# Kernel tuning notes

Measured on AMD Instinct MI355X. Metric: run time of the kernel, lower is better.

The kernel has to match this reference:

```python
import jax, jax.numpy as jnp
import numpy as np

N = 50000      # nodes
E = 1600000    # edges (before self loops)
F = 128        # input_dim
H = 4          # num_heads
D = 32         # hidden_dim (per head)
B = 16         # graphs in batch
NEG_SLOPE = 0.2  # PyG GATv2Conv default negative_slope


def setup_inputs() -> dict:
    key = jax.random.key(0)
    ks = jax.random.split(key, 8)
    x = jax.random.normal(ks[0], (N, F), dtype=jnp.float32)
    edge_index = jax.random.randint(ks[1], (2, E), 0, N, dtype=jnp.int32)
    batch = jnp.sort(jax.random.randint(ks[2], (N,), 0, B, dtype=jnp.int32))
    s = 0.05
    W_l = jax.random.normal(ks[3], (F, H * D), dtype=jnp.float32) * s
    b_l = jnp.zeros((H * D,), dtype=jnp.float32)
    W_r = jax.random.normal(ks[4], (F, H * D), dtype=jnp.float32) * s
    b_r = jnp.zeros((H * D,), dtype=jnp.float32)
    att = jax.random.normal(ks[5], (H, D), dtype=jnp.float32) * s
    bias = jnp.zeros((H * D,), dtype=jnp.float32)
    return {"x": x, "edge_index": edge_index, "batch": batch,
            "W_l": W_l, "b_l": b_l, "W_r": W_r, "b_r": b_r,
            "att": att, "bias": bias}


def reference(x, edge_index, batch, W_l, b_l, W_r, b_r, att, bias):
    n = x.shape[0]
    # PyG GATv2Conv adds self loops by default
    loops = jnp.arange(n, dtype=edge_index.dtype)
    src = jnp.concatenate([edge_index[0], loops])  # message source j
    dst = jnp.concatenate([edge_index[1], loops])  # message target i

    xl = (x @ W_l + b_l).reshape(n, H, D)  # source transform
    xr = (x @ W_r + b_r).reshape(n, H, D)  # target transform

    # per-edge GATv2 attention logits: a^T LeakyReLU(xl_j + xr_i)
    m = xl[src] + xr[dst]                                   # [E+N, H, D]
    e = jnp.sum(jax.nn.leaky_relu(m, NEG_SLOPE) * att, -1)  # [E+N, H]

    # softmax over incoming edges of each destination node
    e_max = jax.ops.segment_max(e, dst, num_segments=n)
    ex = jnp.exp(e - e_max[dst])
    den = jax.ops.segment_sum(ex, dst, num_segments=n)
    alpha = ex / den[dst]                                   # [E+N, H]

    # weighted scatter-sum aggregation of source features
    out = jax.ops.segment_sum(alpha[..., None] * xl[src], dst, num_segments=n)
    out = out.reshape(n, H * D) + bias                      # concat heads + bias
    out = jax.nn.relu(out)

    # global max pool over nodes of each graph
    pooled = jax.ops.segment_max(out, batch, num_segments=B)
    pooled = jnp.where(jnp.isfinite(pooled), pooled, 0.0)   # guard empty graphs
    return pooled
```

## Files before the change

### kernel.cpp

```cpp
#include <hip/hip_runtime.h>

#define NN 50000
#define NE 1600000
#define FDIM 128
#define CDIM 128
#define NGRAPH 16
#define SLOPE 0.2f
#define CSTRIDE 96
#define BINSH 7
#define NBIN 391
#define EPB 6400
#define NB1 250
#define EPT 25
#define CAP 5120
#define POOL_NODES 64
#define POOL_NB ((NN + POOL_NODES - 1) / POOL_NODES)
#define TNB 782

__device__ __forceinline__ unsigned short f2bf(float f) {
    unsigned u = __float_as_uint(f);
    return (unsigned short)((u + 0x7FFFu + ((u >> 16) & 1u)) >> 16);
}
__device__ __forceinline__ unsigned packbf(float a, float b) {
    return (unsigned)f2bf(a) | ((unsigned)f2bf(b) << 16);
}
#define BFLO(u) __uint_as_float((u) << 16)
#define BFHI(u) __uint_as_float((u) & 0xffff0000u)

typedef __attribute__((ext_vector_type(8))) short short8;
typedef __attribute__((ext_vector_type(4))) float f32x4;
union FragU { uint4 u; short8 s; };

__global__ __launch_bounds__(256) void k_init(float* __restrict__ out,
                                              int* __restrict__ gbin_cnt) {
    int i = blockIdx.x * 256 + threadIdx.x;
    if (i < NGRAPH * CDIM) out[i] = 0.f;
    if (i < NBIN) gbin_cnt[i] = 0;
}

__global__ __launch_bounds__(256) void k_front(
    const float* __restrict__ x,
    const float* __restrict__ Wl, const float* __restrict__ bl,
    const float* __restrict__ Wr, const float* __restrict__ br,
    const int* __restrict__ src, const int* __restrict__ dst,
    int* __restrict__ gbin_cnt, unsigned* __restrict__ gstage,
    unsigned short* __restrict__ xlh, float* __restrict__ xr) {
    __shared__ __align__(16) char shraw[32768];
    const int tid = threadIdx.x;

    if (blockIdx.x < NB1) {
        int* bcnt = (int*)shraw;
        int* boff = bcnt + NBIN;
        int* gb   = boff + NBIN;
        int* sc   = gb + NBIN;
        unsigned* st = (unsigned*)(sc + 256);
        const int t  = tid;
        const int e0 = blockIdx.x * EPB;

        for (int b = t; b < NBIN; b += 256) bcnt[b] = 0;
        __syncthreads();

        unsigned sd[EPT]; int bn[EPT]; int pl[EPT];
#pragma unroll
        for (int k = 0; k < EPT; k++) {
            int e = e0 + k * 256 + t;
            int s = src[e], d = dst[e];
            bn[k] = d >> BINSH;
            sd[k] = (unsigned)s | ((unsigned)(d & 127) << 16)
                                | ((unsigned)bn[k] << 23);
            pl[k] = atomicAdd(&bcnt[bn[k]], 1);
        }
        __syncthreads();

        int c0 = (2*t     < NBIN) ? bcnt[2*t]     : 0;
        int c1 = (2*t + 1 < NBIN) ? bcnt[2*t + 1] : 0;
        int v  = c0 + c1;
        sc[t] = v; __syncthreads();
        for (int off = 1; off < 256; off <<= 1) {
            int add = (t >= off) ? sc[t - off] : 0;
            __syncthreads();
            sc[t] += add;
            __syncthreads();
        }
        int base = sc[t] - v;
        if (2*t     < NBIN) boff[2*t]     = base;
        if (2*t + 1 < NBIN) boff[2*t + 1] = base + c0;
        __syncthreads();

        for (int b = t; b < NBIN; b += 256) {
            int c = bcnt[b];
            gb[b] = (c > 0) ? atomicAdd(&gbin_cnt[b], c) : 0;
        }
#pragma unroll
        for (int k = 0; k < EPT; k++) st[boff[bn[k]] + pl[k]] = sd[k];
        __syncthreads();

        for (int idx = t; idx < EPB; idx += 256) {
            unsigned w = st[idx];
            int b = w >> 23;
            int p = gb[b] + (idx - boff[b]);
            if (p < CAP) gstage[(size_t)b * CAP + p] = w;
        }
    } else {
        uint4* wfrag = (uint4*)shraw;
        const int bid   = blockIdx.x - NB1;
        const int wv    = tid >> 6;
        const int lane  = tid & 63;
        const int quad  = lane >> 4;
        const int col   = lane & 15;
        const int node0 = bid * 64;
        const int nodeA = node0 + wv * 16 + col;
        const bool aval = nodeA < NN;

        FragU afrag[4];
#pragma unroll
        for (int kq = 0; kq < 4; kq++) {
            float4 lo = make_float4(0.f,0.f,0.f,0.f), hi = lo;
            if (aval) {
                const float* ap = &x[(size_t)nodeA * FDIM + kq * 32 + quad * 8];
                lo = *(const float4*)ap;
                hi = *(const float4*)(ap + 4);
            }
            afrag[kq].u.x = packbf(lo.x, lo.y);
            afrag[kq].u.y = packbf(lo.z, lo.w);
            afrag[kq].u.z = packbf(hi.x, hi.y);
            afrag[kq].u.w = packbf(hi.z, hi.w);
        }

        const int myrow0 = node0 + wv * 16 + quad * 4;

        for (int mat = 0; mat < 2; mat++) {
            const float* W  = mat ? Wr : Wl;
            const float* bb = mat ? br : bl;
            __syncthreads();
            for (int i = 0; i < 8; i++) {
                int C = i * 256 + tid;
                int ccol = C & 15, cq = (C >> 4) & 3, ckq = (C >> 6) & 3, cnt_ = C >> 8;
                const float* wp = &W[(size_t)(ckq * 32 + cq * 8) * CDIM + cnt_ * 16 + ccol];
                uint4 u;
                u.x = packbf(wp[0],        wp[CDIM]);
                u.y = packbf(wp[2*CDIM],   wp[3*CDIM]);
                u.z = packbf(wp[4*CDIM],   wp[5*CDIM]);
                u.w = packbf(wp[6*CDIM],   wp[7*CDIM]);
                wfrag[C] = u;
            }
            __syncthreads();

#pragma unroll
            for (int nt = 0; nt < 8; nt++) {
                f32x4 acc = {0.f, 0.f, 0.f, 0.f};
#pragma unroll
                for (int kq = 0; kq < 4; kq++) {
                    FragU bfr;
                    bfr.u = wfrag[(nt * 4 + kq) * 64 + lane];
                    acc = __builtin_amdgcn_mfma_f32_16x16x32_bf16(
                              afrag[kq].s, bfr.s, acc, 0, 0, 0);
                }
                int ch = nt * 16 + col;
                float bv = bb[ch];
                if (mat == 0) {
#pragma unroll
                    for (int r = 0; r < 4; r++) {
                        int node = myrow0 + r;
                        if (node < NN)
                            xlh[(size_t)node * CDIM + ch] = f2bf(acc[r] + bv);
                    }
                } else {
#pragma unroll
                    for (int r = 0; r < 4; r++) {
                        int node = myrow0 + r;
                        if (node < NN)
                            xr[(size_t)node * CDIM + ch] = acc[r] + bv;
                    }
                }
            }
        }
    }
}

__global__ __launch_bounds__(512) void k_csr(
    const int* __restrict__ gbin_cnt, const unsigned* __restrict__ gstage,
    int* __restrict__ cnt, unsigned short* __restrict__ colp) {
    __shared__ int nfill[128];
    __shared__ unsigned short crow[128 * CSTRIDE];
    const int bin = blockIdx.x;
    const int t   = threadIdx.x;
    const int n0  = bin << BINSH;
    const int nb  = min(128, NN - n0);
    const int m   = min(gbin_cnt[bin], CAP);

    if (t < 128) nfill[t] = 0;
    __syncthreads();

    unsigned w[10];
    bool     ok[10];
#pragma unroll
    for (int k = 0; k < 10; k++) {
        int i = k * 512 + t;
        ok[k] = i < m;
        if (ok[k]) w[k] = gstage[(size_t)bin * CAP + i];
    }
#pragma unroll
    for (int k = 0; k < 10; k++) {
        if (ok[k]) {
            int dl = (w[k] >> 16) & 127;
            int p  = atomicAdd(&nfill[dl], 1);
            if (p < CSTRIDE - 1)
                crow[dl * CSTRIDE + p] = (unsigned short)(w[k] & 0xFFFF);
        }
    }
    __syncthreads();

    if (t < nb) {
        int c = min(nfill[t], CSTRIDE - 1);
        crow[t * CSTRIDE + c] = (unsigned short)(n0 + t);
        cnt[n0 + t] = c + 1;
    }
    __syncthreads();

    unsigned* gout = (unsigned*)colp + (size_t)bin * (128 * CSTRIDE / 2);
    const unsigned* cin = (const unsigned*)crow;
    for (int idx = t; idx < 128 * CSTRIDE / 2; idx += 512) gout[idx] = cin[idx];
}

__device__ __forceinline__ void edge_body(
    const unsigned short* __restrict__ xlh, int j, int ch0,
    const float4& rx0, const float4& rx1,
    const float4& p0, const float4& p1,
    const float4& q0, const float4& q1,
    float& s, float* acc) {
    uint4 q = *(const uint4*)&xlh[(size_t)j * CDIM + ch0];
    float4 v0 = make_float4(BFLO(q.x), BFHI(q.x), BFLO(q.y), BFHI(q.y));
    float4 v1 = make_float4(BFLO(q.z), BFHI(q.z), BFLO(q.w), BFHI(q.w));
    float t0, d = 0.f;
    t0 = v0.x + rx0.x; d = fmaf(t0, p0.x, d); d = fmaf(fabsf(t0), q0.x, d);
    t0 = v0.y + rx0.y; d = fmaf(t0, p0.y, d); d = fmaf(fabsf(t0), q0.y, d);
    t0 = v0.z + rx0.z; d = fmaf(t0, p0.z, d); d = fmaf(fabsf(t0), q0.z, d);
    t0 = v0.w + rx0.w; d = fmaf(t0, p0.w, d); d = fmaf(fabsf(t0), q0.w, d);
    t0 = v1.x + rx1.x; d = fmaf(t0, p1.x, d); d = fmaf(fabsf(t0), q1.x, d);
    t0 = v1.y + rx1.y; d = fmaf(t0, p1.y, d); d = fmaf(fabsf(t0), q1.y, d);
    t0 = v1.z + rx1.z; d = fmaf(t0, p1.z, d); d = fmaf(fabsf(t0), q1.z, d);
    t0 = v1.w + rx1.w; d = fmaf(t0, p1.w, d); d = fmaf(fabsf(t0), q1.w, d);
    d += __shfl_xor(d, 1);
    d += __shfl_xor(d, 2);
    float w = __expf(d);
    s += w;
    acc[0] = fmaf(w, v0.x, acc[0]);
    acc[1] = fmaf(w, v0.y, acc[1]);
    acc[2] = fmaf(w, v0.z, acc[2]);
    acc[3] = fmaf(w, v0.w, acc[3]);
    acc[4] = fmaf(w, v1.x, acc[4]);
    acc[5] = fmaf(w, v1.y, acc[5]);
    acc[6] = fmaf(w, v1.z, acc[6]);
    acc[7] = fmaf(w, v1.w, acc[7]);
}

__global__ __launch_bounds__(256) void k_aggregate(
    const unsigned short* __restrict__ xlh, const float* __restrict__ xr,
    const float* __restrict__ att, const float* __restrict__ bias,
    const int* __restrict__ cnt, const unsigned short* __restrict__ colp,
    float* __restrict__ nodeout) {
    const int wave = blockIdx.x * 4 + (threadIdx.x >> 6);
    const int lane = threadIdx.x & 63;
    const int i     = wave;
    const size_t start = (size_t)i * CSTRIDE;
    const int deg   = cnt[i];
    const int grp   = lane >> 4;
    const int ch0   = (lane & 15) * 8;

    int cj0 = (int)colp[start + lane];
    int cj1 = 0;
    if (deg > 64) cj1 = (int)colp[start + 64 + lane];

    const float4 rx0 = *(const float4*)&xr[(size_t)i * CDIM + ch0];
    const float4 rx1 = *(const float4*)&xr[(size_t)i * CDIM + ch0 + 4];
    const float4 aa0 = *(const float4*)&att[ch0];
    const float4 aa1 = *(const float4*)&att[ch0 + 4];
    const float4 p0 = make_float4(0.6f*aa0.x, 0.6f*aa0.y, 0.6f*aa0.z, 0.6f*aa0.w);
    const float4 p1 = make_float4(0.6f*aa1.x, 0.6f*aa1.y, 0.6f*aa1.z, 0.6f*aa1.w);
    const float4 q0 = make_float4(0.4f*aa0.x, 0.4f*aa0.y, 0.4f*aa0.z, 0.4f*aa0.w);
    const float4 q1 = make_float4(0.4f*aa1.x, 0.4f*aa1.y, 0.4f*aa1.z, 0.4f*aa1.w);

    float s = 0.f;
    float acc[8];
#pragma unroll
    for (int k = 0; k < 8; k++) acc[k] = 0.f;

    const int full = deg >> 2;
    const int f0   = full < 16 ? full : 16;
#pragma unroll 2
    for (int t = 0; t < f0; t++) {
        int j = __shfl(cj0, t * 4 + grp);
        edge_body(xlh, j, ch0, rx0, rx1, p0, p1, q0, q1, s, acc);
    }
    for (int t = 16; t < full; t++) {
        int j = __shfl(cj1, t * 4 + grp - 64);
        edge_body(xlh, j, ch0, rx0, rx1, p0, p1, q0, q1, s, acc);
    }
    int e  = full * 4 + grp;
    int jt = (e < 64) ? __shfl(cj0, e) : __shfl(cj1, (e - 64) & 63);
    if (e < deg)
        edge_body(xlh, jt, ch0, rx0, rx1, p0, p1, q0, q1, s, acc);

#pragma unroll
    for (int dist = 16; dist <= 32; dist <<= 1) {
        s += __shfl_xor(s, dist);
#pragma unroll
        for (int k = 0; k < 8; k++) acc[k] += __shfl_xor(acc[k], dist);
    }

    if (grp == 0) {
        float inv = 1.f / s;
        float4 o0, o1;
        const float4 b0 = *(const float4*)&bias[ch0];
        const float4 b1 = *(const float4*)&bias[ch0 + 4];
        o0.x = fmaxf(fmaf(acc[0], inv, b0.x), 0.f);
        o0.y = fmaxf(fmaf(acc[1], inv, b0.y), 0.f);
        o0.z = fmaxf(fmaf(acc[2], inv, b0.z), 0.f);
        o0.w = fmaxf(fmaf(acc[3], inv, b0.w), 0.f);
        o1.x = fmaxf(fmaf(acc[4], inv, b1.x), 0.f);
        o1.y = fmaxf(fmaf(acc[5], inv, b1.y), 0.f);
        o1.z = fmaxf(fmaf(acc[6], inv, b1.z), 0.f);
        o1.w = fmaxf(fmaf(acc[7], inv, b1.w), 0.f);
        float* op = &nodeout[(size_t)i * CDIM + ch0];
        *(float4*)op       = o0;
        *(float4*)(op + 4) = o1;
    }
}

__global__ __launch_bounds__(256) void k_pool(
    const float* __restrict__ nodeout, const int* __restrict__ batch,
    float* __restrict__ out) {
    const int tid  = threadIdx.x;
    const int c4   = (tid & 31) * 4;
    const int nl   = tid >> 5;
    const int base = blockIdx.x * POOL_NODES;
    float4 mx = make_float4(0.f, 0.f, 0.f, 0.f);
    int cur = -1;
#pragma unroll
    for (int k = 0; k < POOL_NODES / 8; k++) {
        int node = base + k * 8 + nl;
        if (node >= NN) break;
        int g = batch[node];
        if (g != cur) {
            if (cur >= 0) {
                int* op = (int*)&out[cur * CDIM + c4];
                if (mx.x > 0.f) atomicMax(op,     __float_as_int(mx.x));
                if (mx.y > 0.f) atomicMax(op + 1, __float_as_int(mx.y));
                if (mx.z > 0.f) atomicMax(op + 2, __float_as_int(mx.z));
                if (mx.w > 0.f) atomicMax(op + 3, __float_as_int(mx.w));
            }
            cur = g;
            mx = make_float4(0.f, 0.f, 0.f, 0.f);
        }
        float4 v = *(const float4*)&nodeout[(size_t)node * CDIM + c4];
        mx.x = fmaxf(mx.x, v.x);
        mx.y = fmaxf(mx.y, v.y);
        mx.z = fmaxf(mx.z, v.z);
        mx.w = fmaxf(mx.w, v.w);
    }
    if (cur >= 0) {
        int* op = (int*)&out[cur * CDIM + c4];
        if (mx.x > 0.f) atomicMax(op,     __float_as_int(mx.x));
        if (mx.y > 0.f) atomicMax(op + 1, __float_as_int(mx.y));
        if (mx.z > 0.f) atomicMax(op + 2, __float_as_int(mx.z));
        if (mx.w > 0.f) atomicMax(op + 3, __float_as_int(mx.w));
    }
}

extern "C" void kernel_launch(void* const* d_in, const int* in_sizes, int n_in,
                              void* d_out, int out_size, void* d_ws, size_t ws_size,
                              hipStream_t stream) {
    const float* x     = (const float*)d_in[0];
    const int*   ei    = (const int*)d_in[1];
    const int*   batch = (const int*)d_in[2];
    const float* Wl    = (const float*)d_in[3];
    const float* bl    = (const float*)d_in[4];
    const float* Wr    = (const float*)d_in[5];
    const float* br    = (const float*)d_in[6];
    const float* att   = (const float*)d_in[7];
    const float* bias  = (const float*)d_in[8];
    float* out = (float*)d_out;

    char* w = (char*)d_ws;
    float*          xr       = (float*)w;          w += (size_t)NN * CDIM * 4;
    float*          nodeout  = (float*)w;          w += (size_t)NN * CDIM * 4;
    unsigned short* xlh      = (unsigned short*)w; w += (size_t)NN * CDIM * 2;
    int*            cnt      = (int*)w;            w += (size_t)NN * 4;
    unsigned short* colp     = (unsigned short*)w; w += (size_t)NBIN * 128 * CSTRIDE * 2;
    unsigned*       gstage   = (unsigned*)w;       w += (size_t)NBIN * CAP * 4;
    int*            gbin_cnt = (int*)w;            w += (size_t)NBIN * 4;

    const int* src = ei;
    const int* dst = ei + NE;

    k_init<<<10, 256, 0, stream>>>(out, gbin_cnt);
    k_front<<<NB1 + TNB, 256, 0, stream>>>(x, Wl, bl, Wr, br,
                                           src, dst, gbin_cnt, gstage, xlh, xr);
    k_csr<<<NBIN, 512, 0, stream>>>(gbin_cnt, gstage, cnt, colp);
    k_aggregate<<<NN / 4, 256, 0, stream>>>(xlh, xr, att, bias,
                                            cnt, colp, nodeout);
    k_pool<<<POOL_NB, 256, 0, stream>>>(nodeout, batch, out);
}
```

Before: 229.6 us.

## Store xr and node outputs in bf16, split CSR bins, rebalance binning blocks

Stores the target transform xr and the post-ReLU node outputs as bf16 instead of fp32, which halves the bytes written by the front and aggregate kernels and read by aggregate and pool. The CSR build now uses two blocks per bin, each handling 64 destination rows, to get more parallelism. The edge-binning stage uses more blocks with fewer edges per thread. The change adds bf16 rounding error to the attention logits and to the pooled maxima, and each CSR block now reads the whole bin stage to keep only half of it.

```diff
diff --git a/kernel.cpp b/kernel.cpp
--- a/kernel.cpp
+++ b/kernel.cpp
@@ -9,9 +9,9 @@
 #define CSTRIDE 96
 #define BINSH 7
 #define NBIN 391
-#define EPB 6400
-#define NB1 250
-#define EPT 25
+#define EPB 2560
+#define NB1 625
+#define EPT 10
 #define CAP 5120
 #define POOL_NODES 64
 #define POOL_NB ((NN + POOL_NODES - 1) / POOL_NODES)
@@ -44,7 +44,7 @@
     const float* __restrict__ Wr, const float* __restrict__ br,
     const int* __restrict__ src, const int* __restrict__ dst,
     int* __restrict__ gbin_cnt, unsigned* __restrict__ gstage,
-    unsigned short* __restrict__ xlh, float* __restrict__ xr) {
+    unsigned short* __restrict__ xlh, unsigned short* __restrict__ xrh) {
     __shared__ __align__(16) char shraw[32768];
     const int tid = threadIdx.x;
 
@@ -132,6 +132,7 @@
         for (int mat = 0; mat < 2; mat++) {
             const float* W  = mat ? Wr : Wl;
             const float* bb = mat ? br : bl;
+            unsigned short* dstp = mat ? xrh : xlh;
             __syncthreads();
             for (int i = 0; i < 8; i++) {
                 int C = i * 256 + tid;
@@ -158,20 +159,11 @@
                 }
                 int ch = nt * 16 + col;
                 float bv = bb[ch];
-                if (mat == 0) {
-#pragma unroll
-                    for (int r = 0; r < 4; r++) {
-                        int node = myrow0 + r;
-                        if (node < NN)
-                            xlh[(size_t)node * CDIM + ch] = f2bf(acc[r] + bv);
-                    }
-                } else {
-#pragma unroll
-                    for (int r = 0; r < 4; r++) {
-                        int node = myrow0 + r;
-                        if (node < NN)
-                            xr[(size_t)node * CDIM + ch] = acc[r] + bv;
-                    }
+#pragma unroll
+                for (int r = 0; r < 4; r++) {
+                    int node = myrow0 + r;
+                    if (node < NN)
+                        dstp[(size_t)node * CDIM + ch] = f2bf(acc[r] + bv);
                 }
             }
         }
@@ -181,15 +173,16 @@
 __global__ __launch_bounds__(512) void k_csr(
     const int* __restrict__ gbin_cnt, const unsigned* __restrict__ gstage,
     int* __restrict__ cnt, unsigned short* __restrict__ colp) {
-    __shared__ int nfill[128];
-    __shared__ unsigned short crow[128 * CSTRIDE];
-    const int bin = blockIdx.x;
+    __shared__ int nfill[64];
+    __shared__ unsigned short crow[64 * CSTRIDE];
+    const int bin = blockIdx.x >> 1;
+    const int h   = blockIdx.x & 1;
     const int t   = threadIdx.x;
-    const int n0  = bin << BINSH;
-    const int nb  = min(128, NN - n0);
+    const int n0  = (bin << BINSH) + h * 64;
+    const int nb  = min(64, NN - n0);
     const int m   = min(gbin_cnt[bin], CAP);
 
-    if (t < 128) nfill[t] = 0;
+    if (t < 64) nfill[t] = 0;
     __syncthreads();
 
     unsigned w[10];
@@ -204,9 +197,12 @@
     for (int k = 0; k < 10; k++) {
         if (ok[k]) {
             int dl = (w[k] >> 16) & 127;
-            int p  = atomicAdd(&nfill[dl], 1);
-            if (p < CSTRIDE - 1)
-                crow[dl * CSTRIDE + p] = (unsigned short)(w[k] & 0xFFFF);
+            if ((dl >> 6) == h) {
+                int r = dl & 63;
+                int p = atomicAdd(&nfill[r], 1);
+                if (p < CSTRIDE - 1)
+                    crow[r * CSTRIDE + p] = (unsigned short)(w[k] & 0xFFFF);
+            }
         }
     }
     __syncthreads();
@@ -218,9 +214,9 @@
     }
     __syncthreads();
 
-    unsigned* gout = (unsigned*)colp + (size_t)bin * (128 * CSTRIDE / 2);
+    unsigned* gout = (unsigned*)colp + (size_t)n0 * CSTRIDE / 2;
     const unsigned* cin = (const unsigned*)crow;
-    for (int idx = t; idx < 128 * CSTRIDE / 2; idx += 512) gout[idx] = cin[idx];
+    for (int idx = t; idx < 64 * CSTRIDE / 2; idx += 512) gout[idx] = cin[idx];
 }
 
 __device__ __forceinline__ void edge_body(
@@ -256,10 +252,10 @@
 }
 
 __global__ __launch_bounds__(256) void k_aggregate(
-    const unsigned short* __restrict__ xlh, const float* __restrict__ xr,
+    const unsigned short* __restrict__ xlh, const unsigned short* __restrict__ xrh,
     const float* __restrict__ att, const float* __restrict__ bias,
     const int* __restrict__ cnt, const unsigned short* __restrict__ colp,
-    float* __restrict__ nodeout) {
+    unsigned short* __restrict__ nodeh) {
     const int wave = blockIdx.x * 4 + (threadIdx.x >> 6);
     const int lane = threadIdx.x & 63;
     const int i     = wave;
@@ -272,8 +268,9 @@
     int cj1 = 0;
     if (deg > 64) cj1 = (int)colp[start + 64 + lane];
 
-    const float4 rx0 = *(const float4*)&xr[(size_t)i * CDIM + ch0];
-    const float4 rx1 = *(const float4*)&xr[(size_t)i * CDIM + ch0 + 4];
+    uint4 qr = *(const uint4*)&xrh[(size_t)i * CDIM + ch0];
+    const float4 rx0 = make_float4(BFLO(qr.x), BFHI(qr.x), BFLO(qr.y), BFHI(qr.y));
+    const float4 rx1 = make_float4(BFLO(qr.z), BFHI(qr.z), BFLO(qr.w), BFHI(qr.w));
     const float4 aa0 = *(const float4*)&att[ch0];
     const float4 aa1 = *(const float4*)&att[ch0 + 4];
     const float4 p0 = make_float4(0.6f*aa0.x, 0.6f*aa0.y, 0.6f*aa0.z, 0.6f*aa0.w);
@@ -311,60 +308,59 @@
 
     if (grp == 0) {
         float inv = 1.f / s;
-        float4 o0, o1;
         const float4 b0 = *(const float4*)&bias[ch0];
         const float4 b1 = *(const float4*)&bias[ch0 + 4];
-        o0.x = fmaxf(fmaf(acc[0], inv, b0.x), 0.f);
-        o0.y = fmaxf(fmaf(acc[1], inv, b0.y), 0.f);
-        o0.z = fmaxf(fmaf(acc[2], inv, b0.z), 0.f);
-        o0.w = fmaxf(fmaf(acc[3], inv, b0.w), 0.f);
-        o1.x = fmaxf(fmaf(acc[4], inv, b1.x), 0.f);
-        o1.y = fmaxf(fmaf(acc[5], inv, b1.y), 0.f);
-        o1.z = fmaxf(fmaf(acc[6], inv, b1.z), 0.f);
-        o1.w = fmaxf(fmaf(acc[7], inv, b1.w), 0.f);
-        float* op = &nodeout[(size_t)i * CDIM + ch0];
-        *(float4*)op       = o0;
-        *(float4*)(op + 4) = o1;
+        uint4 o;
+        o.x = packbf(fmaxf(fmaf(acc[0], inv, b0.x), 0.f),
+                     fmaxf(fmaf(acc[1], inv, b0.y), 0.f));
+        o.y = packbf(fmaxf(fmaf(acc[2], inv, b0.z), 0.f),
+                     fmaxf(fmaf(acc[3], inv, b0.w), 0.f));
+        o.z = packbf(fmaxf(fmaf(acc[4], inv, b1.x), 0.f),
+                     fmaxf(fmaf(acc[5], inv, b1.y), 0.f));
+        o.w = packbf(fmaxf(fmaf(acc[6], inv, b1.z), 0.f),
+                     fmaxf(fmaf(acc[7], inv, b1.w), 0.f));
+        *(uint4*)&nodeh[(size_t)i * CDIM + ch0] = o;
     }
 }
 
 __global__ __launch_bounds__(256) void k_pool(
-    const float* __restrict__ nodeout, const int* __restrict__ batch,
+    const unsigned short* __restrict__ nodeh, const int* __restrict__ batch,
     float* __restrict__ out) {
     const int tid  = threadIdx.x;
-    const int c4   = (tid & 31) * 4;
-    const int nl   = tid >> 5;
+    const int ch0  = (tid & 15) * 8;
+    const int nl   = tid >> 4;
     const int base = blockIdx.x * POOL_NODES;
-    float4 mx = make_float4(0.f, 0.f, 0.f, 0.f);
+    float mx[8];
+#pragma unroll
+    for (int k = 0; k < 8; k++) mx[k] = 0.f;
     int cur = -1;
 #pragma unroll
-    for (int k = 0; k < POOL_NODES / 8; k++) {
-        int node = base + k * 8 + nl;
+    for (int k = 0; k < POOL_NODES / 16; k++) {
+        int node = base + k * 16 + nl;
         if (node >= NN) break;
         int g = batch[node];
         if (g != cur) {
             if (cur >= 0) {
-                int* op = (int*)&out[cur * CDIM + c4];
-                if (mx.x > 0.f) atomicMax(op,     __float_as_int(mx.x));
-                if (mx.y > 0.f) atomicMax(op + 1, __float_as_int(mx.y));
-                if (mx.z > 0.f) atomicMax(op + 2, __float_as_int(mx.z));
-                if (mx.w > 0.f) atomicMax(op + 3, __float_as_int(mx.w));
+                int* op = (int*)&out[cur * CDIM + ch0];
+#pragma unroll
+                for (int j = 0; j < 8; j++)
+                    if (mx[j] > 0.f) atomicMax(op + j, __float_as_int(mx[j]));
             }
             cur = g;
-            mx = make_float4(0.f, 0.f, 0.f, 0.f);
-        }
-        float4 v = *(const float4*)&nodeout[(size_t)node * CDIM + c4];
-        mx.x = fmaxf(mx.x, v.x);
-        mx.y = fmaxf(mx.y, v.y);
-        mx.z = fmaxf(mx.z, v.z);
-        mx.w = fmaxf(mx.w, v.w);
+#pragma unroll
+            for (int j = 0; j < 8; j++) mx[j] = 0.f;
+        }
+        uint4 q = *(const uint4*)&nodeh[(size_t)node * CDIM + ch0];
+        mx[0] = fmaxf(mx[0], BFLO(q.x)); mx[1] = fmaxf(mx[1], BFHI(q.x));
+        mx[2] = fmaxf(mx[2], BFLO(q.y)); mx[3] = fmaxf(mx[3], BFHI(q.y));
+        mx[4] = fmaxf(mx[4], BFLO(q.z)); mx[5] = fmaxf(mx[5], BFHI(q.z));
+        mx[6] = fmaxf(mx[6], BFLO(q.w)); mx[7] = fmaxf(mx[7], BFHI(q.w));
     }
     if (cur >= 0) {
-        int* op = (int*)&out[cur * CDIM + c4];
-        if (mx.x > 0.f) atomicMax(op,     __float_as_int(mx.x));
-        if (mx.y > 0.f) atomicMax(op + 1, __float_as_int(mx.y));
-        if (mx.z > 0.f) atomicMax(op + 2, __float_as_int(mx.z));
-        if (mx.w > 0.f) atomicMax(op + 3, __float_as_int(mx.w));
+        int* op = (int*)&out[cur * CDIM + ch0];
+#pragma unroll
+        for (int j = 0; j < 8; j++)
+            if (mx[j] > 0.f) atomicMax(op + j, __float_as_int(mx[j]));
     }
 }
 
@@ -383,9 +379,9 @@
     float* out = (float*)d_out;
 
     char* w = (char*)d_ws;
-    float*          xr       = (float*)w;          w += (size_t)NN * CDIM * 4;
-    float*          nodeout  = (float*)w;          w += (size_t)NN * CDIM * 4;
     unsigned short* xlh      = (unsigned short*)w; w += (size_t)NN * CDIM * 2;
+    unsigned short* xrh      = (unsigned short*)w; w += (size_t)NN * CDIM * 2;
+    unsigned short* nodeh    = (unsigned short*)w; w += (size_t)NN * CDIM * 2;
     int*            cnt      = (int*)w;            w += (size_t)NN * 4;
     unsigned short* colp     = (unsigned short*)w; w += (size_t)NBIN * 128 * CSTRIDE * 2;
     unsigned*       gstage   = (unsigned*)w;       w += (size_t)NBIN * CAP * 4;
@@ -396,9 +392,9 @@
 
     k_init<<<10, 256, 0, stream>>>(out, gbin_cnt);
     k_front<<<NB1 + TNB, 256, 0, stream>>>(x, Wl, bl, Wr, br,
-                                           src, dst, gbin_cnt, gstage, xlh, xr);
-    k_csr<<<NBIN, 512, 0, stream>>>(gbin_cnt, gstage, cnt, colp);
-    k_aggregate<<<NN / 4, 256, 0, stream>>>(xlh, xr, att, bias,
-                                            cnt, colp, nodeout);
-    k_pool<<<POOL_NB, 256, 0, stream>>>(nodeout, batch, out);
-}
+                                           src, dst, gbin_cnt, gstage, xlh, xrh);
+    k_csr<<<NBIN * 2, 512, 0, stream>>>(gbin_cnt, gstage, cnt, colp);
+    k_aggregate<<<NN / 4, 256, 0, stream>>>(xlh, xrh, att, bias,
+                                            cnt, colp, nodeh);
+    k_pool<<<POOL_NB, 256, 0, stream>>>(nodeh, batch, out);
+}
```

Result: slower. 376.6 us (+64.0%).
